# Performance work log

Hardware: AMD Instinct MI355X
Metric: run time of the kernel (lower is better)

The kernel has to match this reference:

```python
import jax, jax.numpy as jnp
import numpy as np

B, CIN, COUT, K = 16, 64, 64, 3
H = W = 192
DEG, HID = 64, 256


def setup_inputs() -> dict:
    key = jax.random.key(0)
    ks = jax.random.split(key, 6)
    x = jax.random.normal(ks[0], (B, CIN, H, W), dtype=jnp.float32)
    degradation_features = jax.random.normal(ks[1], (B, DEG), dtype=jnp.float32)
    # weight_generator: Linear(DEG,256) -> ReLU -> Linear(256, CIN*COUT*K*K)
    W1 = jax.random.normal(ks[2], (DEG, HID), dtype=jnp.float32) * (1.0 / np.sqrt(DEG))
    b1 = jax.random.normal(ks[3], (HID,), dtype=jnp.float32) * 0.01
    W2 = jax.random.normal(ks[4], (HID, CIN * COUT * K * K), dtype=jnp.float32) * (1.0 / np.sqrt(HID))
    b2 = jax.random.normal(ks[5], (CIN * COUT * K * K,), dtype=jnp.float32) * 0.01
    return {"x": x, "degradation_features": degradation_features,
            "W1": W1, "b1": b1, "W2": W2, "b2": b2}


def _forward(x, degradation_features, W1, b1, W2, b2):
    # generate per-sample conv weights: [B, COUT, CIN, K, K] (OIHW)
    h = jax.nn.relu(degradation_features @ W1 + b1)
    weights = (h @ W2 + b2).reshape(B, COUT, CIN, K, K)

    # Per-sample conv2d, NO padding (original loop omits padding arg -> VALID).
    def conv_one(xi, wi):
        # xi: [CIN, H, W], wi: [COUT, CIN, K, K]
        out = jax.lax.conv_general_dilated(
            xi[None], wi, window_strides=(1, 1), padding='VALID',
            dimension_numbers=('NCHW', 'OIHW', 'NCHW'))
        return out[0]  # [COUT, H-K+1, W-K+1]

    return jax.vmap(conv_one)(x, weights)


def reference(x, degradation_features, W1, b1, W2, b2):
    return _forward(x, degradation_features, W1, b1, W2, b2)
```

## Files before the change

kernel.cpp:

```cpp
#include <hip/hip_runtime.h>


typedef __bf16 bf16x8 __attribute__((ext_vector_type(8)));
typedef float  f32x4  __attribute__((ext_vector_type(4)));

#define NB   16
#define CIN  64
#define COUT 64
#define HW   192
#define OHW  190
#define NPIX (HW*HW)
#define NW2  (COUT*CIN*9)

__device__ __forceinline__ unsigned short f2bf(float f) {
    union { float f; unsigned int u; } v; v.f = f;
    unsigned int r = v.u + 0x7FFFu + ((v.u >> 16) & 1u);
    return (unsigned short)(r >> 16);
}

__device__ __forceinline__ void async_copy16(const void* gsrc, void* ldst) {
    __builtin_amdgcn_global_load_lds(
        (const __attribute__((address_space(1))) unsigned int*)gsrc,
        (__attribute__((address_space(3))) unsigned int*)ldst, 16, 0, 0);
}

__global__ __launch_bounds__(256)
void k23(const float* __restrict__ x, unsigned short* __restrict__ xT,
         const float* __restrict__ deg, const float* __restrict__ W1,
         const float* __restrict__ b1, const float* __restrict__ W2,
         const float* __restrict__ b2, unsigned short* __restrict__ Aw) {
    __shared__ __align__(16) char smem[37376];
    const int bid = blockIdx.x;
    const int t   = threadIdx.x;

    if (bid < 9216) {
        float (*tile)[65] = (float (*)[65])smem;
        int b  = bid / 576;
        int p0 = (bid - b*576) * 64;
        const float* xb = x + (size_t)b * CIN * NPIX;
        {
            int c  = (t & 15) * 4;
            int r0 = t >> 4;
            #pragma unroll
            for (int i = 0; i < 4; ++i) {
                int ci = r0 + 16*i;
                float4 v = *(const float4*)(xb + (size_t)ci*NPIX + p0 + c);
                tile[ci][c] = v.x; tile[ci][c+1] = v.y; tile[ci][c+2] = v.z; tile[ci][c+3] = v.w;
            }
        }
        __syncthreads();
        {
            int ci8 = (t & 7) * 8;
            int pr0 = t >> 3;
            #pragma unroll
            for (int i = 0; i < 2; ++i) {
                int pl = pr0 + 32*i;
                union { uint4 v; unsigned short u[8]; } pk;
                #pragma unroll
                for (int j = 0; j < 8; ++j) pk.u[j] = f2bf(tile[ci8 + j][pl]);
                *(uint4*)(&xT[((size_t)b*NPIX + p0 + pl)*CIN + ci8]) = pk.v;
            }
        }
    } else {
        float* degs = (float*)smem;
        float* hs   = degs + 16*64;
        float (*red)[16][33] = (float (*)[16][33])(hs + 16*256);
        int nb = bid - 9216;

        for (int i = t; i < 16*64; i += 256) degs[i] = deg[i];
        __syncthreads();
        {
            float acc[16];
            float bias = b1[t];
            #pragma unroll
            for (int bb2 = 0; bb2 < 16; ++bb2) acc[bb2] = bias;
            for (int d = 0; d < 64; ++d) {
                float w = W1[d*256 + t];
                #pragma unroll
                for (int bb2 = 0; bb2 < 16; ++bb2) acc[bb2] += degs[bb2*64 + d] * w;
            }
            #pragma unroll
            for (int bb2 = 0; bb2 < 16; ++bb2) hs[bb2*256 + t] = fmaxf(acc[bb2], 0.f);
        }
        __syncthreads();

        int nl = t & 31;
        int kc = t >> 5;
        int n  = nb * 32 + nl;
        float acc[16] = {};
        #pragma unroll
        for (int kk = 0; kk < 32; ++kk) {
            int k = kc*32 + kk;
            float w = W2[(size_t)k*NW2 + n];
            #pragma unroll
            for (int b = 0; b < 16; ++b) acc[b] += hs[b*256 + k] * w;
        }
        #pragma unroll
        for (int b = 0; b < 16; ++b) red[kc][b][nl] = acc[b];
        __syncthreads();

        for (int i = t; i < 512; i += 256) {
            int b  = i >> 5;
            int nn = i & 31;
            int n2 = nb * 32 + nn;
            float s = b2[n2];
            #pragma unroll
            for (int k = 0; k < 8; ++k) s += red[k][b][nn];
            int co  = n2 / 576;
            int rem = n2 - co*576;
            int ci  = rem / 9;
            int tap = rem - ci*9;
            Aw[(((b*9 + tap)*COUT + co)*CIN) + ci] = f2bf(s);
        }
    }
}

#define XS_SLOTS 2816
__global__ __launch_bounds__(256, 3)
void k4_conv(const unsigned short* __restrict__ xT, const unsigned short* __restrict__ Aw,
             float* __restrict__ out) {
    __shared__ unsigned short xs[XS_SLOTS*8];
    const int tid = threadIdx.x;

    int bid = blockIdx.x;
    int wg  = (bid & 7) * 288 + (bid >> 3);
    int b   = wg / 144;
    int ry  = wg - b*144;
    int ty  = ry / 6;
    int tx  = ry - ty*6;
    const int x0 = tx * 32;
    const int y0 = ty * 8;

    const int wv  = tid >> 6;
    const int l   = tid & 63;
    const int l15 = l & 15;
    const int lg  = l >> 4;

    const unsigned short* xTb = xT + (size_t)b * NPIX * CIN;
    #pragma unroll
    for (int it = 0; it < 11; ++it) {
        int s   = it*256 + tid;
        int t   = s >> 3;
        int swc = s & 7;
        int gyl = t / 34;
        int gxl = t - gyl*34;
        int gy  = y0 + gyl; gy = gy > 191 ? 191 : gy;
        int gx  = x0 + gxl; gx = gx > 191 ? 191 : gx;
        const void* src = xTb + ((size_t)(gy*HW + gx))*CIN + ((swc ^ (gx & 7)) * 8);
        void* dst = &xs[(it*256 + wv*64) * 8];
        async_copy16(src, dst);
    }

    const unsigned short* Ab = Aw + b * (9*COUT*CIN);
    const unsigned short* Al = Ab + l15*CIN + lg*8;
    bf16x8 a[2][8];
    #pragma unroll
    for (int cc = 0; cc < 2; ++cc)
        #pragma unroll
        for (int m = 0; m < 4; ++m)
            a[0][cc*4+m] = *(const bf16x8*)(Al + m*1024 + cc*32);

    __syncthreads();

    f32x4 acc[4][4] = {};

    #pragma unroll
    for (int tap = 0; tap < 9; ++tap) {
        const int cur = tap & 1, nxt = cur ^ 1;
        if (tap < 8) {
            #pragma unroll
            for (int cc = 0; cc < 2; ++cc)
                #pragma unroll
                for (int m = 0; m < 4; ++m)
                    a[nxt][cc*4+m] = *(const bf16x8*)(Al + (tap+1)*4096 + m*1024 + cc*32);
        }
        const int ky = tap / 3, kx = tap - 3*(tap/3);
        #pragma unroll
        for (int cc = 0; cc < 2; ++cc) {
            bf16x8 bb[4];
            #pragma unroll
            for (int r = 0; r < 2; ++r)
                #pragma unroll
                for (int xb = 0; xb < 2; ++xb) {
                    int gyl = 2*wv + r + ky;
                    int gxl = xb*16 + l15 + kx;
                    int pch = (cc*4 + lg) ^ (gxl & 7);
                    bb[r*2 + xb] = *(const bf16x8*)(&xs[((gyl*34 + gxl)*8 + pch)*8]);
                }
            __builtin_amdgcn_s_setprio(1);
            #pragma unroll
            for (int m = 0; m < 4; ++m)
                #pragma unroll
                for (int n = 0; n < 4; ++n)
                    acc[m][n] = __builtin_amdgcn_mfma_f32_16x16x32_bf16(a[cur][cc*4+m], bb[n], acc[m][n], 0, 0, 0);
            __builtin_amdgcn_s_setprio(0);
        }
    }

    #pragma unroll
    for (int m = 0; m < 4; ++m)
        #pragma unroll
        for (int r = 0; r < 2; ++r)
            #pragma unroll
            for (int xb = 0; xb < 2; ++xb) {
                int oy = y0 + 2*wv + r;
                int ox = x0 + xb*16 + l15;
                if (oy < OHW && ox < OHW) {
                    f32x4 v = acc[m][r*2 + xb];
                    #pragma unroll
                    for (int j = 0; j < 4; ++j) {
                        int co = m*16 + lg*4 + j;
                        out[((size_t)(b*COUT + co)*OHW + oy)*OHW + ox] = v[j];
                    }
                }
            }
}

extern "C" void kernel_launch(void* const* d_in, const int* in_sizes, int n_in,
                              void* d_out, int out_size, void* d_ws, size_t ws_size,
                              hipStream_t stream) {
    const float* x   = (const float*)d_in[0];
    const float* deg = (const float*)d_in[1];
    const float* W1  = (const float*)d_in[2];
    const float* b1  = (const float*)d_in[3];
    const float* W2  = (const float*)d_in[4];
    const float* b2  = (const float*)d_in[5];
    float* out = (float*)d_out;

    unsigned short* Aw = (unsigned short*)d_ws;
    unsigned short* xT = (unsigned short*)((char*)d_ws + (size_t)NB*9*COUT*CIN*2);

    k23<<<9216 + 1152, 256, 0, stream>>>(x, xT, deg, W1, b1, W2, b2, Aw);
    k4_conv<<<2304, 256, 0, stream>>>(xT, Aw, out);
}
```

Before: 189.2 us.

## Drop LDS staging in conv; load input rows directly and reuse across ky taps

The conv kernel no longer stages the input tile into shared memory with async copies. Each wave now loads its four input rows straight from global memory into registers and reuses each loaded row fragment across the three ky taps. The loop is reordered over (cc, kx) with double-buffered weight registers that each hold all ky taps. This removes the LDS round trip and the block barrier, but raises register pressure and puts more uncoalesced global and L2 traffic in the MFMA loop.

```diff
diff --git a/kernel.cpp b/kernel.cpp
--- a/kernel.cpp
+++ b/kernel.cpp
@@ -16,12 +16,6 @@
     union { float f; unsigned int u; } v; v.f = f;
     unsigned int r = v.u + 0x7FFFu + ((v.u >> 16) & 1u);
     return (unsigned short)(r >> 16);
-}
-
-__device__ __forceinline__ void async_copy16(const void* gsrc, void* ldst) {
-    __builtin_amdgcn_global_load_lds(
-        (const __attribute__((address_space(1))) unsigned int*)gsrc,
-        (__attribute__((address_space(3))) unsigned int*)ldst, 16, 0, 0);
 }
 
 __global__ __launch_bounds__(256)
@@ -115,11 +109,9 @@
     }
 }
 
-#define XS_SLOTS 2816
 __global__ __launch_bounds__(256, 3)
 void k4_conv(const unsigned short* __restrict__ xT, const unsigned short* __restrict__ Aw,
              float* __restrict__ out) {
-    __shared__ unsigned short xs[XS_SLOTS*8];
     const int tid = threadIdx.x;
 
     int bid = blockIdx.x;
@@ -137,64 +129,63 @@
     const int lg  = l >> 4;
 
     const unsigned short* xTb = xT + (size_t)b * NPIX * CIN;
-    #pragma unroll
-    for (int it = 0; it < 11; ++it) {
-        int s   = it*256 + tid;
-        int t   = s >> 3;
-        int swc = s & 7;
-        int gyl = t / 34;
-        int gxl = t - gyl*34;
-        int gy  = y0 + gyl; gy = gy > 191 ? 191 : gy;
-        int gx  = x0 + gxl; gx = gx > 191 ? 191 : gx;
-        const void* src = xTb + ((size_t)(gy*HW + gx))*CIN + ((swc ^ (gx & 7)) * 8);
-        void* dst = &xs[(it*256 + wv*64) * 8];
-        async_copy16(src, dst);
+    const unsigned short* Al  = Aw + b*(9*COUT*CIN) + l15*CIN + lg*8;
+
+    const unsigned short* rowp[4];
+    #pragma unroll
+    for (int q = 0; q < 4; ++q) {
+        int gy = y0 + 2*wv + q; if (gy > 191) gy = 191;
+        rowp[q] = xTb + (size_t)gy * HW * CIN;
     }
 
-    const unsigned short* Ab = Aw + b * (9*COUT*CIN);
-    const unsigned short* Al = Ab + l15*CIN + lg*8;
-    bf16x8 a[2][8];
-    #pragma unroll
-    for (int cc = 0; cc < 2; ++cc)
+    f32x4 acc[4][4] = {};
+
+    bf16x8 aA[12], aB[12];
+    #pragma unroll
+    for (int ky = 0; ky < 3; ++ky)
         #pragma unroll
         for (int m = 0; m < 4; ++m)
-            a[0][cc*4+m] = *(const bf16x8*)(Al + m*1024 + cc*32);
-
-    __syncthreads();
-
-    f32x4 acc[4][4] = {};
-
-    #pragma unroll
-    for (int tap = 0; tap < 9; ++tap) {
-        const int cur = tap & 1, nxt = cur ^ 1;
-        if (tap < 8) {
-            #pragma unroll
-            for (int cc = 0; cc < 2; ++cc)
-                #pragma unroll
-                for (int m = 0; m < 4; ++m)
-                    a[nxt][cc*4+m] = *(const bf16x8*)(Al + (tap+1)*4096 + m*1024 + cc*32);
-        }
-        const int ky = tap / 3, kx = tap - 3*(tap/3);
-        #pragma unroll
-        for (int cc = 0; cc < 2; ++cc) {
-            bf16x8 bb[4];
-            #pragma unroll
-            for (int r = 0; r < 2; ++r)
-                #pragma unroll
-                for (int xb = 0; xb < 2; ++xb) {
-                    int gyl = 2*wv + r + ky;
-                    int gxl = xb*16 + l15 + kx;
-                    int pch = (cc*4 + lg) ^ (gxl & 7);
-                    bb[r*2 + xb] = *(const bf16x8*)(&xs[((gyl*34 + gxl)*8 + pch)*8]);
-                }
-            __builtin_amdgcn_s_setprio(1);
+            aA[ky*4+m] = *(const bf16x8*)(Al + (ky*3 + 0)*4096 + m*1024 + 0*32);
+
+    #pragma unroll
+    for (int st = 0; st < 6; ++st) {
+        const int cc = st / 3, kx = st - 3*(st/3);
+        if (st < 5) {
+            const int ns = st + 1;
+            const int ncc = ns / 3, nkx = ns - 3*(ns/3);
+            if (st & 1) {
+                #pragma unroll
+                for (int ky = 0; ky < 3; ++ky)
+                    #pragma unroll
+                    for (int m = 0; m < 4; ++m)
+                        aA[ky*4+m] = *(const bf16x8*)(Al + (ky*3 + nkx)*4096 + m*1024 + ncc*32);
+            } else {
+                #pragma unroll
+                for (int ky = 0; ky < 3; ++ky)
+                    #pragma unroll
+                    for (int m = 0; m < 4; ++m)
+                        aB[ky*4+m] = *(const bf16x8*)(Al + (ky*3 + nkx)*4096 + m*1024 + ncc*32);
+            }
+        }
+        bf16x8 bb[4][2];
+        #pragma unroll
+        for (int q = 0; q < 4; ++q)
+            #pragma unroll
+            for (int xb = 0; xb < 2; ++xb) {
+                int gx = x0 + xb*16 + l15 + kx; if (gx > 191) gx = 191;
+                bb[q][xb] = *(const bf16x8*)(rowp[q] + (size_t)gx*CIN + cc*32 + lg*8);
+            }
+        #pragma unroll
+        for (int ky = 0; ky < 3; ++ky)
             #pragma unroll
             for (int m = 0; m < 4; ++m)
                 #pragma unroll
-                for (int n = 0; n < 4; ++n)
-                    acc[m][n] = __builtin_amdgcn_mfma_f32_16x16x32_bf16(a[cur][cc*4+m], bb[n], acc[m][n], 0, 0, 0);
-            __builtin_amdgcn_s_setprio(0);
-        }
+                for (int r = 0; r < 2; ++r)
+                    #pragma unroll
+                    for (int xb = 0; xb < 2; ++xb)
+                        acc[m][r*2+xb] = __builtin_amdgcn_mfma_f32_16x16x32_bf16(
+                            (st & 1) ? aB[ky*4+m] : aA[ky*4+m],
+                            bb[ky+r][xb], acc[m][r*2+xb], 0, 0, 0);
     }
 
     #pragma unroll
@@ -206,7 +197,7 @@
                 int oy = y0 + 2*wv + r;
                 int ox = x0 + xb*16 + l15;
                 if (oy < OHW && ox < OHW) {
-                    f32x4 v = acc[m][r*2 + xb];
+                    f32x4 v = acc[m][r*2+xb];
                     #pragma unroll
                     for (int j = 0; j < 4; ++j) {
                         int co = m*16 + lg*4 + j;
```

Result: slower. 242.3 us (+28.1%).
